# Optimization experiments

Hardware: AMD Instinct MI355X
Metric: run time of the kernel (lower is better)

The kernel has to match this reference:

```python
import jax, jax.numpy as jnp
import numpy as np

N_EMB = 1024
HEAD_SIZE = 64
BLOCK_SIZE = 2048
B, T = 8, 2048


def setup_inputs() -> dict:
    key = jax.random.key(0)
    kx, kq, kk, kv = jax.random.split(key, 4)
    scale = 1.0 / (N_EMB ** 0.5)
    x = jax.random.normal(kx, (B, T, N_EMB), dtype=jnp.float32)
    Wq = jax.random.uniform(kq, (N_EMB, HEAD_SIZE), dtype=jnp.float32) * scale
    Wk = jax.random.uniform(kk, (N_EMB, HEAD_SIZE), dtype=jnp.float32) * scale
    Wv = jax.random.uniform(kv, (N_EMB, HEAD_SIZE), dtype=jnp.float32) * scale
    return {"x": x, "Wq": Wq, "Wk": Wk, "Wv": Wv}


def reference(x, Wq, Wk, Wv):
    # Faithful to Head.__call__ with is_training=False.
    # NOTE: original code applies NO 1/sqrt(head_size) scaling to the scores.
    Bt, Tt, _ = x.shape
    q = x @ Wq                      # (B, T, H)
    k = x @ Wk                      # (B, T, H)
    v = x @ Wv                      # (B, T, H)
    wei = jnp.einsum('bth,bsh->bts', q, k)  # (B, T, T)
    causal = jnp.tril(jnp.ones((Tt, Tt), dtype=bool))
    wei = jnp.where(causal, wei, -jnp.inf)
    wei = jax.nn.softmax(wei, axis=-1)
    out = jnp.einsum('bts,bsh->bth', wei, v)  # (B, T, H)
    return out
```

## Files before the change

### kernel.cpp

```cpp
#include <hip/hip_runtime.h>
#include <hip/hip_bf16.h>

#define BB 8
#define TT 2048
#define EE 1024
#define HH 64

typedef __attribute__((ext_vector_type(8))) short short8;
typedef __attribute__((ext_vector_type(4))) float f32x4;

__device__ inline f32x4 mfma_16x16x32(short8 a, short8 b, f32x4 c) {
  return __builtin_amdgcn_mfma_f32_16x16x32_bf16(a, b, c, 0, 0, 0);
}

__device__ inline void gload_lds16(const __hip_bfloat16* g, __hip_bfloat16* l) {
  __builtin_amdgcn_global_load_lds((const __attribute__((address_space(1))) void*)g,
                                   (__attribute__((address_space(3))) void*)l,
                                   16, 0, 0);
}

__device__ inline short f2bf(float f) {
  __hip_bfloat16 h = __float2bfloat16(f);
  return *reinterpret_cast<short*>(&h);
}
__device__ inline float bf2f(short s) {
  __hip_bfloat16 h = *reinterpret_cast<__hip_bfloat16*>(&s);
  return __bfloat162float(h);
}

#define WAIT_LGKM0() __builtin_amdgcn_s_waitcnt(0xC07F)

__global__ void prep_w(const float* __restrict__ Wq, const float* __restrict__ Wk,
                       const float* __restrict__ Wv,
                       __hip_bfloat16* __restrict__ Wthi,
                       __hip_bfloat16* __restrict__ Wtlo,
                       float* __restrict__ maxk2) {
  const int n = blockIdx.x;
  if (n == 0 && threadIdx.x < 8) maxk2[threadIdx.x] = 0.f;
  const int m = n >> 6;
  const int h = n & 63;
  const float* W = (m == 0) ? Wq : (m == 1) ? Wk : Wv;
  const int e0 = threadIdx.x * 4;
#pragma unroll
  for (int j = 0; j < 4; ++j) {
    const float w = W[(e0 + j) * 64 + h];
    const __hip_bfloat16 hi = __float2bfloat16(w);
    Wthi[n * 1024 + e0 + j] = hi;
    Wtlo[n * 1024 + e0 + j] = __float2bfloat16(w - __bfloat162float(hi));
  }
}

__global__ __launch_bounds__(256) void qkv_gemm(
    const float* __restrict__ x,
    const __hip_bfloat16* __restrict__ Wthi, const __hip_bfloat16* __restrict__ Wtlo,
    __hip_bfloat16* __restrict__ qhi, __hip_bfloat16* __restrict__ qlo,
    __hip_bfloat16* __restrict__ khi, __hip_bfloat16* __restrict__ klo,
    __hip_bfloat16* __restrict__ vT) {
  __shared__ __hip_bfloat16 Ahi[2][32 * 72];
  __shared__ __hip_bfloat16 Alo[2][32 * 72];
  __shared__ __hip_bfloat16 Bhi[2][192 * 64];

  const int tid  = threadIdx.x;
  const int wave = tid >> 6;
  const int lane = tid & 63;
  const int row0 = blockIdx.x * 32;
  const int l15 = lane & 15, l4 = lane >> 4;

  const int lr = tid >> 3;
  const int le = (tid & 7) * 8;
  const float* xrow = x + (row0 + lr) * 1024 + le;

  f32x4 acc[2][3];
#pragma unroll
  for (int m = 0; m < 2; ++m)
#pragma unroll
    for (int j = 0; j < 3; ++j) acc[m][j] = f32x4{0.f, 0.f, 0.f, 0.f};

  auto issue_Bhi = [&](int c, int buf) {
    const int g = (lane & 7) ^ ((lane >> 3) & 7);
#pragma unroll
    for (int s = 0; s < 3; ++s) {
      const int j = wave + s * 4;
#pragma unroll
      for (int qh = 0; qh < 2; ++qh) {
        const int qq = j * 2 + qh;
        const int n  = qq * 8 + (lane >> 3);
        gload_lds16(Wthi + n * 1024 + c * 64 + g * 8, &Bhi[buf][qq * 512]);
      }
    }
  };
  auto load_Blo = [&](int c, short8* bl) {
#pragma unroll
    for (int jj = 0; jj < 2; ++jj) {
      const int j = wave + jj * 4;
      const __hip_bfloat16* p = Wtlo + (j * 16 + l15) * 1024 + c * 64;
      bl[jj * 2]     = *(const short8*)(p + l4 * 8);
      bl[jj * 2 + 1] = *(const short8*)(p + 32 + l4 * 8);
    }
  };
  auto write_A = [&](int buf, const f32x4* xr) {
    short8 h0, l0;
    const float* xf = (const float*)xr;
#pragma unroll
    for (int j = 0; j < 8; ++j) {
      const float v = xf[j];
      const short h = f2bf(v);
      h0[j] = h;
      l0[j] = f2bf(v - bf2f(h));
    }
    *(short8*)&Ahi[buf][lr * 72 + le] = h0;
    *(short8*)&Alo[buf][lr * 72 + le] = l0;
  };
  auto compute = [&](int buf, const short8* bl) {
#pragma unroll
    for (int m = 0; m < 2; ++m) {
      const int tr = m * 16 + l15;
      short8 ah0 = *(const short8*)&Ahi[buf][tr * 72 + l4 * 8];
      short8 ah1 = *(const short8*)&Ahi[buf][tr * 72 + 32 + l4 * 8];
      short8 al0 = *(const short8*)&Alo[buf][tr * 72 + l4 * 8];
      short8 al1 = *(const short8*)&Alo[buf][tr * 72 + 32 + l4 * 8];
#pragma unroll
      for (int jj = 0; jj < 3; ++jj) {
        const int j  = (jj < 2) ? (wave + jj * 4) : (wave + 8);
        const int n  = j * 16 + l15;
        const int o0 = ((l4)     ^ (n & 7)) * 8;
        const int o1 = ((4 + l4) ^ (n & 7)) * 8;
        short8 bh0 = *(const short8*)&Bhi[buf][n * 64 + o0];
        short8 bh1 = *(const short8*)&Bhi[buf][n * 64 + o1];
        acc[m][jj] = mfma_16x16x32(ah0, bh0, acc[m][jj]);
        acc[m][jj] = mfma_16x16x32(ah1, bh1, acc[m][jj]);
        if (jj < 2) {
          acc[m][jj] = mfma_16x16x32(ah0, bl[jj * 2],     acc[m][jj]);
          acc[m][jj] = mfma_16x16x32(ah1, bl[jj * 2 + 1], acc[m][jj]);
          acc[m][jj] = mfma_16x16x32(al0, bh0, acc[m][jj]);
          acc[m][jj] = mfma_16x16x32(al1, bh1, acc[m][jj]);
        }
      }
    }
  };

  f32x4 xr[2], xn[2];
  {
    const f32x4* p = (const f32x4*)xrow;
    xr[0] = p[0]; xr[1] = p[1];
  }
  short8 blc[4], bln[4];
  issue_Bhi(0, 0);
  load_Blo(0, blc);
  __builtin_amdgcn_s_waitcnt(0);
  write_A(0, xr);
  __syncthreads();

  for (int c = 0; c < 16; ++c) {
    const int p = c & 1;
    if (c < 15) {
      const f32x4* pp = (const f32x4*)(xrow + (c + 1) * 64);
      xn[0] = pp[0]; xn[1] = pp[1];
      issue_Bhi(c + 1, p ^ 1);
      load_Blo(c + 1, bln);
    }
    compute(p, blc);
    if (c < 15) {
      __builtin_amdgcn_s_waitcnt(0);
      write_A(p ^ 1, xn);
#pragma unroll
      for (int q = 0; q < 4; ++q) blc[q] = bln[q];
    }
    __syncthreads();
  }

  const int hcol = wave * 16 + l15;
#pragma unroll
  for (int jj = 0; jj < 3; ++jj) {
#pragma unroll
    for (int m = 0; m < 2; ++m) {
#pragma unroll
      for (int r = 0; r < 4; ++r) {
        const int trow = row0 + m * 16 + l4 * 4 + r;
        const float val = acc[m][jj][r];
        if (jj == 0) {
          const __hip_bfloat16 hi = __float2bfloat16(val);
          qhi[trow * 64 + hcol] = hi;
          qlo[trow * 64 + hcol] = __float2bfloat16(val - __bfloat162float(hi));
        } else if (jj == 1) {
          const __hip_bfloat16 hi = __float2bfloat16(val);
          khi[trow * 64 + hcol] = hi;
          klo[trow * 64 + hcol] = __float2bfloat16(val - __bfloat162float(hi));
        } else {
          const int bb = trow >> 11, tl = trow & 2047;
          vT[(bb * 64 + hcol) * 2048 + tl] = __float2bfloat16(val);
        }
      }
    }
  }
}

__global__ __launch_bounds__(256) void knorm(
    const __hip_bfloat16* __restrict__ khi, const __hip_bfloat16* __restrict__ klo,
    float* __restrict__ maxk2) {
  const int row = blockIdx.x * 256 + threadIdx.x;
  const int b = row >> 11;
  const __hip_bfloat16* ph = khi + row * 64;
  const __hip_bfloat16* pl = klo + row * 64;
  float s = 0.f;
#pragma unroll
  for (int i = 0; i < 8; ++i) {
    const short8 h = *(const short8*)(ph + i * 8);
    const short8 l = *(const short8*)(pl + i * 8);
#pragma unroll
    for (int j = 0; j < 8; ++j) {
      const float v = bf2f(h[j]) + bf2f(l[j]);
      s += v * v;
    }
  }
  for (int off = 1; off < 64; off <<= 1) s = fmaxf(s, __shfl_xor(s, off));
  if ((threadIdx.x & 63) == 0)
    atomicMax((int*)&maxk2[b], __float_as_int(s));
}

__global__ __launch_bounds__(256, 2) void attn(
    const __hip_bfloat16* __restrict__ qhi, const __hip_bfloat16* __restrict__ qlo,
    const __hip_bfloat16* __restrict__ khi, const __hip_bfloat16* __restrict__ klo,
    const __hip_bfloat16* __restrict__ vT, const float* __restrict__ maxk2,
    float* __restrict__ out) {
  __shared__ __hip_bfloat16 Psm[4][2][16 * 72];
  __shared__ float Osm[4][32][65];
  __shared__ float Lsm[4][32];

  const int tid  = threadIdx.x;
  const int wave = tid >> 6;
  const int lane = tid & 63;
  const int l15 = lane & 15, l4 = lane >> 4;

  const int b = blockIdx.x & 7;
  const int g = blockIdx.x >> 3;
  const int ss = (g < 32) ? (63 - g) : (g - 32);
  const int t0 = ss * 32;
  const int ntiles = (ss >> 1) + 1;

  short8 qh0[2], qh1[2], ql0[2], ql1[2];
#pragma unroll
  for (int m = 0; m < 2; ++m) {
    const __hip_bfloat16* qph = qhi + (b * 2048 + t0 + m * 16 + l15) * 64;
    const __hip_bfloat16* qpl = qlo + (b * 2048 + t0 + m * 16 + l15) * 64;
    qh0[m] = *(const short8*)(qph + l4 * 8);
    qh1[m] = *(const short8*)(qph + 32 + l4 * 8);
    ql0[m] = *(const short8*)(qpl + l4 * 8);
    ql1[m] = *(const short8*)(qpl + 32 + l4 * 8);
  }

  const float kmax = sqrtf(maxk2[b]);
  float c_[2][4];
#pragma unroll
  for (int m = 0; m < 2; ++m) {
    float qn = 0.f;
#pragma unroll
    for (int i = 0; i < 8; ++i) {
      const float v0 = bf2f(qh0[m][i]) + bf2f(ql0[m][i]);
      const float v1 = bf2f(qh1[m][i]) + bf2f(ql1[m][i]);
      qn += v0 * v0 + v1 * v1;
    }
    qn += __shfl_xor(qn, 16);
    qn += __shfl_xor(qn, 32);
    const float crow = sqrtf(qn) * kmax + 2.0f;
#pragma unroll
    for (int r = 0; r < 4; ++r) c_[m][r] = __shfl(crow, l4 * 4 + r);
  }

  short8 ones;
#pragma unroll
  for (int i = 0; i < 8; ++i) ones[i] = (short)0x3F80;

  f32x4 acc[2][4];
#pragma unroll
  for (int m = 0; m < 2; ++m)
#pragma unroll
    for (int j = 0; j < 4; ++j) acc[m][j] = f32x4{0.f, 0.f, 0.f, 0.f};
  f32x4 accL[2];
  accL[0] = f32x4{0.f, 0.f, 0.f, 0.f};
  accL[1] = f32x4{0.f, 0.f, 0.f, 0.f};

  const __hip_bfloat16* kbase_h = khi + (size_t)b * 2048 * 64;
  const __hip_bfloat16* kbase_l = klo + (size_t)b * 2048 * 64;
  const __hip_bfloat16* vbase   = vT + (size_t)b * 64 * 2048;

  short8 kh0[4], kh1[4], kl0[4], kl1[4];
  auto load_K = [&](int k0) {
#pragma unroll
    for (int j = 0; j < 4; ++j) {
      const __hip_bfloat16* kph = kbase_h + (k0 + j * 16 + l15) * 64;
      const __hip_bfloat16* kpl = kbase_l + (k0 + j * 16 + l15) * 64;
      kh0[j] = *(const short8*)(kph + l4 * 8);
      kh1[j] = *(const short8*)(kph + 32 + l4 * 8);
      kl0[j] = *(const short8*)(kpl + l4 * 8);
      kl1[j] = *(const short8*)(kpl + 32 + l4 * 8);
    }
  };

  if (wave < ntiles) load_K(wave << 6);

  for (int kt = wave; kt < ntiles; kt += 4) {
    const int k0 = kt << 6;
    const bool diag = (kt == ntiles - 1);

    f32x4 s_[4];
#pragma unroll
    for (int m = 0; m < 2; ++m) {
      const int rowmax = t0 + m * 16 + 15;
#pragma unroll
      for (int j = 0; j < 4; ++j) {
        if (diag && (k0 + j * 16) > rowmax) {
          s_[j] = f32x4{-1e30f, -1e30f, -1e30f, -1e30f};
        } else {
          f32x4 z = f32x4{0.f, 0.f, 0.f, 0.f};
          z = mfma_16x16x32(qh0[m], kh0[j], z);
          z = mfma_16x16x32(qh1[m], kh1[j], z);
          z = mfma_16x16x32(qh0[m], kl0[j], z);
          z = mfma_16x16x32(qh1[m], kl1[j], z);
          z = mfma_16x16x32(ql0[m], kh0[j], z);
          z = mfma_16x16x32(ql1[m], kh1[j], z);
          s_[j] = z;
        }
      }
      if (m == 1) break;
      if (diag) {
#pragma unroll
        for (int j = 0; j < 4; ++j) {
          const int key = k0 + j * 16 + l15;
#pragma unroll
          for (int r = 0; r < 4; ++r)
            if (key > (t0 + l4 * 4 + r)) s_[j][r] = -1e30f;
        }
      }
#pragma unroll
      for (int j = 0; j < 4; ++j)
#pragma unroll
        for (int r = 0; r < 4; ++r) {
          const float pv = __expf(s_[j][r] - c_[0][r]);
          Psm[wave][0][(l4 * 4 + r) * 72 + j * 16 + l15] = __float2bfloat16(pv);
        }
    }

    short8 vf0[4], vf1[4];
#pragma unroll
    for (int j = 0; j < 4; ++j) {
      const __hip_bfloat16* vp = vbase + (j * 16 + l15) * 2048 + k0;
      vf0[j] = *(const short8*)(vp + l4 * 8);
      vf1[j] = *(const short8*)(vp + 32 + l4 * 8);
    }
    if (kt + 4 < ntiles) load_K((kt + 4) << 6);

    if (diag) {
#pragma unroll
      for (int j = 0; j < 4; ++j) {
        const int key = k0 + j * 16 + l15;
#pragma unroll
        for (int r = 0; r < 4; ++r)
          if (key > (t0 + 16 + l4 * 4 + r)) s_[j][r] = -1e30f;
      }
    }
#pragma unroll
    for (int j = 0; j < 4; ++j)
#pragma unroll
      for (int r = 0; r < 4; ++r) {
        const float pv = __expf(s_[j][r] - c_[1][r]);
        Psm[wave][1][(l4 * 4 + r) * 72 + j * 16 + l15] = __float2bfloat16(pv);
      }

    WAIT_LGKM0();

#pragma unroll
    for (int m = 0; m < 2; ++m) {
      const short8 pf0 = *(const short8*)&Psm[wave][m][l15 * 72 + l4 * 8];
      const short8 pf1 = *(const short8*)&Psm[wave][m][l15 * 72 + 32 + l4 * 8];
#pragma unroll
      for (int j = 0; j < 4; ++j) {
        acc[m][j] = mfma_16x16x32(pf0, vf0[j], acc[m][j]);
        acc[m][j] = mfma_16x16x32(pf1, vf1[j], acc[m][j]);
      }
      accL[m] = mfma_16x16x32(pf0, ones, accL[m]);
      accL[m] = mfma_16x16x32(pf1, ones, accL[m]);
    }
  }

#pragma unroll
  for (int m = 0; m < 2; ++m) {
#pragma unroll
    for (int j = 0; j < 4; ++j)
#pragma unroll
      for (int r = 0; r < 4; ++r)
        Osm[wave][m * 16 + l4 * 4 + r][j * 16 + l15] = acc[m][j][r];
    if (l15 == 0) {
#pragma unroll
      for (int r = 0; r < 4; ++r)
        Lsm[wave][m * 16 + l4 * 4 + r] = accL[m][r];
    }
  }
  __syncthreads();

#pragma unroll
  for (int rr = 0; rr < 8; ++rr) {
    const int row = wave * 8 + rr;
    const float L = Lsm[0][row] + Lsm[1][row] + Lsm[2][row] + Lsm[3][row];
    const float O = Osm[0][row][lane] + Osm[1][row][lane] +
                    Osm[2][row][lane] + Osm[3][row][lane];
    out[(b * 2048 + t0 + row) * 64 + lane] = O / L;
  }
}

extern "C" void kernel_launch(void* const* d_in, const int* in_sizes, int n_in,
                              void* d_out, int out_size, void* d_ws, size_t ws_size,
                              hipStream_t stream) {
  const float* x  = (const float*)d_in[0];
  const float* Wq = (const float*)d_in[1];
  const float* Wk = (const float*)d_in[2];
  const float* Wv = (const float*)d_in[3];
  float* out = (float*)d_out;

  char* ws = (char*)d_ws;
  __hip_bfloat16* Wthi = (__hip_bfloat16*)ws;
  __hip_bfloat16* Wtlo = (__hip_bfloat16*)(ws + 393216);
  __hip_bfloat16* qhi  = (__hip_bfloat16*)(ws + 786432);
  __hip_bfloat16* qlo  = (__hip_bfloat16*)(ws + 786432 + 1 * 2097152);
  __hip_bfloat16* khi  = (__hip_bfloat16*)(ws + 786432 + 2 * 2097152);
  __hip_bfloat16* klo  = (__hip_bfloat16*)(ws + 786432 + 3 * 2097152);
  __hip_bfloat16* vT   = (__hip_bfloat16*)(ws + 786432 + 4 * 2097152);
  float* maxk2         = (float*)(ws + 786432 + 5 * 2097152);

  prep_w<<<192, 256, 0, stream>>>(Wq, Wk, Wv, Wthi, Wtlo, maxk2);
  qkv_gemm<<<512, 256, 0, stream>>>(x, Wthi, Wtlo, qhi, qlo, khi, klo, vT);
  knorm<<<64, 256, 0, stream>>>(khi, klo, maxk2);
  attn<<<512, 256, 0, stream>>>(qhi, qlo, khi, klo, vT, maxk2, out);
}
```

Measured before the change: 162.6 us.

## Drop LDS staging in QKV GEMM and fuse key-norm max into it

The QKV projection kernel stops staging x and the weights in shared memory. Each lane now loads its MFMA operands straight from global memory into registers and splits fp32 x into bf16 hi/lo in registers, with a two-deep register double buffer and no per-chunk barriers. The separate knorm kernel is removed. The per-row squared key norm is computed from the fp32 accumulators with shuffles and reduced per block into the batch max by atomicMax. This saves a launch and the re-read of k, but increases redundant global/L2 traffic because each wave reloads x rows, and raises register pressure under launch_bounds(256,2).

```diff
diff --git a/kernel.cpp b/kernel.cpp
--- a/kernel.cpp
+++ b/kernel.cpp
@@ -11,12 +11,6 @@
 
 __device__ inline f32x4 mfma_16x16x32(short8 a, short8 b, f32x4 c) {
   return __builtin_amdgcn_mfma_f32_16x16x32_bf16(a, b, c, 0, 0, 0);
-}
-
-__device__ inline void gload_lds16(const __hip_bfloat16* g, __hip_bfloat16* l) {
-  __builtin_amdgcn_global_load_lds((const __attribute__((address_space(1))) void*)g,
-                                   (__attribute__((address_space(3))) void*)l,
-                                   16, 0, 0);
 }
 
 __device__ inline short f2bf(float f) {
@@ -50,25 +44,27 @@
   }
 }
 
-__global__ __launch_bounds__(256) void qkv_gemm(
+__global__ __launch_bounds__(256, 2) void qkv_gemm(
     const float* __restrict__ x,
     const __hip_bfloat16* __restrict__ Wthi, const __hip_bfloat16* __restrict__ Wtlo,
     __hip_bfloat16* __restrict__ qhi, __hip_bfloat16* __restrict__ qlo,
     __hip_bfloat16* __restrict__ khi, __hip_bfloat16* __restrict__ klo,
-    __hip_bfloat16* __restrict__ vT) {
-  __shared__ __hip_bfloat16 Ahi[2][32 * 72];
-  __shared__ __hip_bfloat16 Alo[2][32 * 72];
-  __shared__ __hip_bfloat16 Bhi[2][192 * 64];
+    __hip_bfloat16* __restrict__ vT, float* __restrict__ maxk2) {
+  __shared__ float Ksm[4][32];
 
   const int tid  = threadIdx.x;
   const int wave = tid >> 6;
   const int lane = tid & 63;
+  const int l15 = lane & 15, l4 = lane >> 4;
   const int row0 = blockIdx.x * 32;
-  const int l15 = lane & 15, l4 = lane >> 4;
-
-  const int lr = tid >> 3;
-  const int le = (tid & 7) * 8;
-  const float* xrow = x + (row0 + lr) * 1024 + le;
+
+  const __hip_bfloat16* bq_h = Wthi + ((wave)     * 16 + l15) * 1024;
+  const __hip_bfloat16* bk_h = Wthi + ((wave + 4) * 16 + l15) * 1024;
+  const __hip_bfloat16* bv_h = Wthi + ((wave + 8) * 16 + l15) * 1024;
+  const __hip_bfloat16* bq_l = Wtlo + ((wave)     * 16 + l15) * 1024;
+  const __hip_bfloat16* bk_l = Wtlo + ((wave + 4) * 16 + l15) * 1024;
+  const float* xr0 = x + (size_t)(row0 + l15) * 1024;
+  const float* xr1 = x + (size_t)(row0 + 16 + l15) * 1024;
 
   f32x4 acc[2][3];
 #pragma unroll
@@ -76,97 +72,87 @@
 #pragma unroll
     for (int j = 0; j < 3; ++j) acc[m][j] = f32x4{0.f, 0.f, 0.f, 0.f};
 
-  auto issue_Bhi = [&](int c, int buf) {
-    const int g = (lane & 7) ^ ((lane >> 3) & 7);
-#pragma unroll
-    for (int s = 0; s < 3; ++s) {
-      const int j = wave + s * 4;
-#pragma unroll
-      for (int qh = 0; qh < 2; ++qh) {
-        const int qq = j * 2 + qh;
-        const int n  = qq * 8 + (lane >> 3);
-        gload_lds16(Wthi + n * 1024 + c * 64 + g * 8, &Bhi[buf][qq * 512]);
-      }
+  auto load_A = [&](int c, f32x4* xa) {
+#pragma unroll
+    for (int m = 0; m < 2; ++m) {
+      const float* base = (m ? xr1 : xr0) + c * 64 + l4 * 8;
+      xa[m * 4 + 0] = *(const f32x4*)(base);
+      xa[m * 4 + 1] = *(const f32x4*)(base + 4);
+      xa[m * 4 + 2] = *(const f32x4*)(base + 32);
+      xa[m * 4 + 3] = *(const f32x4*)(base + 36);
     }
   };
-  auto load_Blo = [&](int c, short8* bl) {
-#pragma unroll
-    for (int jj = 0; jj < 2; ++jj) {
-      const int j = wave + jj * 4;
-      const __hip_bfloat16* p = Wtlo + (j * 16 + l15) * 1024 + c * 64;
-      bl[jj * 2]     = *(const short8*)(p + l4 * 8);
-      bl[jj * 2 + 1] = *(const short8*)(p + 32 + l4 * 8);
-    }
+  auto load_B = [&](int c, short8* bh, short8* bl) {
+    const int e0 = c * 64 + l4 * 8;
+    bh[0] = *(const short8*)(bq_h + e0);
+    bh[1] = *(const short8*)(bq_h + e0 + 32);
+    bh[2] = *(const short8*)(bk_h + e0);
+    bh[3] = *(const short8*)(bk_h + e0 + 32);
+    bh[4] = *(const short8*)(bv_h + e0);
+    bh[5] = *(const short8*)(bv_h + e0 + 32);
+    bl[0] = *(const short8*)(bq_l + e0);
+    bl[1] = *(const short8*)(bq_l + e0 + 32);
+    bl[2] = *(const short8*)(bk_l + e0);
+    bl[3] = *(const short8*)(bk_l + e0 + 32);
   };
-  auto write_A = [&](int buf, const f32x4* xr) {
-    short8 h0, l0;
-    const float* xf = (const float*)xr;
-#pragma unroll
-    for (int j = 0; j < 8; ++j) {
-      const float v = xf[j];
-      const short h = f2bf(v);
-      h0[j] = h;
-      l0[j] = f2bf(v - bf2f(h));
-    }
-    *(short8*)&Ahi[buf][lr * 72 + le] = h0;
-    *(short8*)&Alo[buf][lr * 72 + le] = l0;
+  auto step = [&](const f32x4* xa, const short8* bh, const short8* bl) {
+    short8 ah[4], al[4];
+#pragma unroll
+    for (int m = 0; m < 2; ++m)
+#pragma unroll
+      for (int h = 0; h < 2; ++h) {
+        short8 hi, lo;
+#pragma unroll
+        for (int i = 0; i < 4; ++i) {
+          const float v = xa[m * 4 + h * 2][i];
+          const short hh = f2bf(v);
+          hi[i] = hh;
+          lo[i] = f2bf(v - bf2f(hh));
+        }
+#pragma unroll
+        for (int i = 0; i < 4; ++i) {
+          const float v = xa[m * 4 + h * 2 + 1][i];
+          const short hh = f2bf(v);
+          hi[4 + i] = hh;
+          lo[4 + i] = f2bf(v - bf2f(hh));
+        }
+        ah[m * 2 + h] = hi;
+        al[m * 2 + h] = lo;
+      }
+#pragma unroll
+    for (int m = 0; m < 2; ++m) {
+      acc[m][0] = mfma_16x16x32(ah[m * 2 + 0], bh[0], acc[m][0]);
+      acc[m][0] = mfma_16x16x32(ah[m * 2 + 1], bh[1], acc[m][0]);
+      acc[m][0] = mfma_16x16x32(ah[m * 2 + 0], bl[0], acc[m][0]);
+      acc[m][0] = mfma_16x16x32(ah[m * 2 + 1], bl[1], acc[m][0]);
+      acc[m][0] = mfma_16x16x32(al[m * 2 + 0], bh[0], acc[m][0]);
+      acc[m][0] = mfma_16x16x32(al[m * 2 + 1], bh[1], acc[m][0]);
+      acc[m][1] = mfma_16x16x32(ah[m * 2 + 0], bh[2], acc[m][1]);
+      acc[m][1] = mfma_16x16x32(ah[m * 2 + 1], bh[3], acc[m][1]);
+      acc[m][1] = mfma_16x16x32(ah[m * 2 + 0], bl[2], acc[m][1]);
+      acc[m][1] = mfma_16x16x32(ah[m * 2 + 1], bl[3], acc[m][1]);
+      acc[m][1] = mfma_16x16x32(al[m * 2 + 0], bh[2], acc[m][1]);
+      acc[m][1] = mfma_16x16x32(al[m * 2 + 1], bh[3], acc[m][1]);
+      acc[m][2] = mfma_16x16x32(ah[m * 2 + 0], bh[4], acc[m][2]);
+      acc[m][2] = mfma_16x16x32(ah[m * 2 + 1], bh[5], acc[m][2]);
+    }
   };
-  auto compute = [&](int buf, const short8* bl) {
-#pragma unroll
-    for (int m = 0; m < 2; ++m) {
-      const int tr = m * 16 + l15;
-      short8 ah0 = *(const short8*)&Ahi[buf][tr * 72 + l4 * 8];
-      short8 ah1 = *(const short8*)&Ahi[buf][tr * 72 + 32 + l4 * 8];
-      short8 al0 = *(const short8*)&Alo[buf][tr * 72 + l4 * 8];
-      short8 al1 = *(const short8*)&Alo[buf][tr * 72 + 32 + l4 * 8];
-#pragma unroll
-      for (int jj = 0; jj < 3; ++jj) {
-        const int j  = (jj < 2) ? (wave + jj * 4) : (wave + 8);
-        const int n  = j * 16 + l15;
-        const int o0 = ((l4)     ^ (n & 7)) * 8;
-        const int o1 = ((4 + l4) ^ (n & 7)) * 8;
-        short8 bh0 = *(const short8*)&Bhi[buf][n * 64 + o0];
-        short8 bh1 = *(const short8*)&Bhi[buf][n * 64 + o1];
-        acc[m][jj] = mfma_16x16x32(ah0, bh0, acc[m][jj]);
-        acc[m][jj] = mfma_16x16x32(ah1, bh1, acc[m][jj]);
-        if (jj < 2) {
-          acc[m][jj] = mfma_16x16x32(ah0, bl[jj * 2],     acc[m][jj]);
-          acc[m][jj] = mfma_16x16x32(ah1, bl[jj * 2 + 1], acc[m][jj]);
-          acc[m][jj] = mfma_16x16x32(al0, bh0, acc[m][jj]);
-          acc[m][jj] = mfma_16x16x32(al1, bh1, acc[m][jj]);
-        }
-      }
-    }
-  };
-
-  f32x4 xr[2], xn[2];
-  {
-    const f32x4* p = (const f32x4*)xrow;
-    xr[0] = p[0]; xr[1] = p[1];
-  }
-  short8 blc[4], bln[4];
-  issue_Bhi(0, 0);
-  load_Blo(0, blc);
-  __builtin_amdgcn_s_waitcnt(0);
-  write_A(0, xr);
-  __syncthreads();
-
-  for (int c = 0; c < 16; ++c) {
-    const int p = c & 1;
-    if (c < 15) {
-      const f32x4* pp = (const f32x4*)(xrow + (c + 1) * 64);
-      xn[0] = pp[0]; xn[1] = pp[1];
-      issue_Bhi(c + 1, p ^ 1);
-      load_Blo(c + 1, bln);
-    }
-    compute(p, blc);
-    if (c < 15) {
-      __builtin_amdgcn_s_waitcnt(0);
-      write_A(p ^ 1, xn);
-#pragma unroll
-      for (int q = 0; q < 4; ++q) blc[q] = bln[q];
-    }
-    __syncthreads();
+
+  f32x4 xa0_[8], xa1_[8];
+  short8 bh0_[6], bh1_[6], bl0_[4], bl1_[4];
+  load_A(0, xa0_);
+  load_B(0, bh0_, bl0_);
+#pragma unroll
+  for (int cc = 0; cc < 8; ++cc) {
+    const int c0 = cc * 2, c1 = c0 + 1;
+    load_A(c1, xa1_);
+    load_B(c1, bh1_, bl1_);
+    step(xa0_, bh0_, bl0_);
+    if (c1 < 15) {
+      load_A(c1 + 1, xa0_);
+      load_B(c1 + 1, bh0_, bl0_);
+    }
+    step(xa1_, bh1_, bl1_);
   }
 
   const int hcol = wave * 16 + l15;
@@ -193,29 +179,27 @@
       }
     }
   }
-}
-
-__global__ __launch_bounds__(256) void knorm(
-    const __hip_bfloat16* __restrict__ khi, const __hip_bfloat16* __restrict__ klo,
-    float* __restrict__ maxk2) {
-  const int row = blockIdx.x * 256 + threadIdx.x;
-  const int b = row >> 11;
-  const __hip_bfloat16* ph = khi + row * 64;
-  const __hip_bfloat16* pl = klo + row * 64;
-  float s = 0.f;
-#pragma unroll
-  for (int i = 0; i < 8; ++i) {
-    const short8 h = *(const short8*)(ph + i * 8);
-    const short8 l = *(const short8*)(pl + i * 8);
-#pragma unroll
-    for (int j = 0; j < 8; ++j) {
-      const float v = bf2f(h[j]) + bf2f(l[j]);
-      s += v * v;
-    }
-  }
-  for (int off = 1; off < 64; off <<= 1) s = fmaxf(s, __shfl_xor(s, off));
-  if ((threadIdx.x & 63) == 0)
-    atomicMax((int*)&maxk2[b], __float_as_int(s));
+
+#pragma unroll
+  for (int m = 0; m < 2; ++m)
+#pragma unroll
+    for (int r = 0; r < 4; ++r) {
+      float s2 = acc[m][1][r] * acc[m][1][r];
+      s2 += __shfl_xor(s2, 1);
+      s2 += __shfl_xor(s2, 2);
+      s2 += __shfl_xor(s2, 4);
+      s2 += __shfl_xor(s2, 8);
+      if (l15 == 0) Ksm[wave][m * 16 + l4 * 4 + r] = s2;
+    }
+  __syncthreads();
+  if (wave == 0) {
+    const int row = lane & 31;
+    float k2 = Ksm[0][row] + Ksm[1][row] + Ksm[2][row] + Ksm[3][row];
+#pragma unroll
+    for (int off = 1; off < 64; off <<= 1) k2 = fmaxf(k2, __shfl_xor(k2, off));
+    if (lane == 0)
+      atomicMax((int*)&maxk2[row0 >> 11], __float_as_int(k2));
+  }
 }
 
 __global__ __launch_bounds__(256, 2) void attn(
@@ -428,7 +412,6 @@
   float* maxk2         = (float*)(ws + 786432 + 5 * 2097152);
 
   prep_w<<<192, 256, 0, stream>>>(Wq, Wk, Wv, Wthi, Wtlo, maxk2);
-  qkv_gemm<<<512, 256, 0, stream>>>(x, Wthi, Wtlo, qhi, qlo, khi, klo, vT);
-  knorm<<<64, 256, 0, stream>>>(khi, klo, maxk2);
+  qkv_gemm<<<512, 256, 0, stream>>>(x, Wthi, Wtlo, qhi, qlo, khi, klo, vT, maxk2);
   attn<<<512, 256, 0, stream>>>(qhi, qlo, khi, klo, vT, maxk2, out);
 }
```

New measurement: 185.8 us. 1.14x slower.
